# Kernel optimization log

Hardware: AMD Instinct MI355X
Metric: run time of the kernel (lower is better)

## Reference

```python
import jax, jax.numpy as jnp
import numpy as np

L, H, D, F = 6, 8, 512, 2048
B, T, S = 8, 512, 1024
DK = D // H


def setup_inputs() -> dict:
    key = jax.random.key(0)
    ks = jax.random.split(key, 16)
    p = lambda k, shape: jax.random.normal(k, shape, jnp.float32) * 0.02
    inp = {
        "tgt": jax.random.normal(ks[0], (B, T, D), jnp.float32),
        "memory": jax.random.normal(ks[1], (B, S, D), jnp.float32),
        "source_mask": jnp.ones((B, 1, 1, S), jnp.int32),
        "target_mask": jnp.broadcast_to(jnp.tril(jnp.ones((T, T), jnp.int32)), (B, 1, T, T)),
        # self-attention params, stacked over layers
        "sa_wq": p(ks[2], (L, D, D)), "sa_wk": p(ks[3], (L, D, D)),
        "sa_wv": p(ks[4], (L, D, D)), "sa_wo": p(ks[5], (L, D, D)),
        "sa_bq": jnp.zeros((L, D)), "sa_bk": jnp.zeros((L, D)),
        "sa_bv": jnp.zeros((L, D)), "sa_bo": jnp.zeros((L, D)),
        # cross-attention params
        "ca_wq": p(ks[6], (L, D, D)), "ca_wk": p(ks[7], (L, D, D)),
        "ca_wv": p(ks[8], (L, D, D)), "ca_wo": p(ks[9], (L, D, D)),
        "ca_bq": jnp.zeros((L, D)), "ca_bk": jnp.zeros((L, D)),
        "ca_bv": jnp.zeros((L, D)), "ca_bo": jnp.zeros((L, D)),
        # FFN params
        "ff_w1": p(ks[10], (L, D, F)), "ff_b1": jnp.zeros((L, F)),
        "ff_w2": p(ks[11], (L, F, D)), "ff_b2": jnp.zeros((L, D)),
        # single shared LayerNorm (as in the original module)
        "ln_g": jnp.ones((D,)), "ln_b": jnp.zeros((D,)),
    }
    return inp


def _layernorm(x, g, b, eps=1e-5):
    m = jnp.mean(x, axis=-1, keepdims=True)
    v = jnp.var(x, axis=-1, keepdims=True)
    return (x - m) * jax.lax.rsqrt(v + eps) * g + b


def _mha(xq, xk, xv, wq, bq, wk, bk, wv, bv, wo, bo, mask):
    Bq = xq.shape[0]
    proj = lambda x, w, b: (x @ w + b).reshape(Bq, -1, H, DK).transpose(0, 2, 1, 3)
    q, k, v = proj(xq, wq, bq), proj(xk, wk, bk), proj(xv, wv, bv)  # [B,H,*,DK]
    scores = jnp.einsum('bhtd,bhsd->bhts', q, k) / jnp.sqrt(jnp.float32(DK))
    scores = jnp.where(mask == 0, jnp.float32(-1e9), scores)
    p_attn = jax.nn.softmax(scores, axis=-1)
    o = jnp.einsum('bhts,bhsd->bhtd', p_attn, v)
    o = o.transpose(0, 2, 1, 3).reshape(Bq, -1, H * DK)
    return o @ wo + bo


def reference(tgt, memory, source_mask, target_mask,
              sa_wq, sa_wk, sa_wv, sa_wo, sa_bq, sa_bk, sa_bv, sa_bo,
              ca_wq, ca_wk, ca_wv, ca_wo, ca_bq, ca_bk, ca_bv, ca_bo,
              ff_w1, ff_b1, ff_w2, ff_b2, ln_g, ln_b):
    output = tgt
    for i in range(L):
        # NOTE: faithful to original code: self-attn block uses `tgt`, not `output`
        n = _layernorm(tgt, ln_g, ln_b)
        output = tgt + _mha(n, n, n,
                            sa_wq[i], sa_bq[i], sa_wk[i], sa_bk[i],
                            sa_wv[i], sa_bv[i], sa_wo[i], sa_bo[i], target_mask)
        n = _layernorm(output, ln_g, ln_b)
        output = output + _mha(n, memory, memory,
                               ca_wq[i], ca_bq[i], ca_wk[i], ca_bk[i],
                               ca_wv[i], ca_bv[i], ca_wo[i], ca_bo[i], source_mask)
        n = _layernorm(output, ln_g, ln_b)
        ff = jax.nn.relu(n @ ff_w1[i] + ff_b1[i]) @ ff_w2[i] + ff_b2[i]
        output = output + ff
    return _layernorm(output, ln_g, ln_b)
```

## Files before the change

kernel.cpp:

```cpp
#include <hip/hip_runtime.h>

typedef __bf16 bf16;
typedef unsigned short u16;
typedef __bf16 bf16x8 __attribute__((ext_vector_type(8)));
typedef __bf16 bf16x4 __attribute__((ext_vector_type(4)));
typedef float f32x4 __attribute__((ext_vector_type(4)));

#define GLL16(gp, lp)                                                        \
    __builtin_amdgcn_global_load_lds(                                        \
        (const __attribute__((address_space(1))) void*)(gp),                 \
        (__attribute__((address_space(3))) void*)(lp), 16, 0, 0)

__device__ __forceinline__ bool is_f32(const void* lng_raw) {
    return ((const unsigned int*)lng_raw)[0] == 0x3F800000u;
}

__device__ __forceinline__ float ldf(const void* base, size_t idx, bool f32) {
    return f32 ? ((const float*)base)[idx] : (float)((const bf16*)base)[idx];
}

__device__ __forceinline__ uint4 load8(const void* base, size_t idx, bool f) {
    if (!f) return *(const uint4*)((const bf16*)base + idx);
    const float* p = (const float*)base + idx;
    float4 a = ((const float4*)p)[0], b = ((const float4*)p)[1];
    union { uint4 u; bf16 h[8]; } r;
    r.h[0] = (bf16)a.x; r.h[1] = (bf16)a.y; r.h[2] = (bf16)a.z; r.h[3] = (bf16)a.w;
    r.h[4] = (bf16)b.x; r.h[5] = (bf16)b.y; r.h[6] = (bf16)b.z; r.h[7] = (bf16)b.w;
    return r.u;
}

struct SrcList { const void* p[10]; };
struct DstList { u16* p[10]; };
struct VecList { const void* p[12]; };
__global__ __launch_bounds__(256) void prep_all_k(SrcList SL, DstList DL, VecList VL,
                                                  bf16* __restrict__ cvec,
                                                  const void* __restrict__ mem,
                                                  bf16* __restrict__ membf,
                                                  const void* __restrict__ tgt,
                                                  bf16* __restrict__ nbuf) {
    __shared__ u16 tile[32][33];
    const void* lng_raw = VL.p[10];
    const void* lnb_raw = VL.p[11];
    bool f = is_f32(lng_raw);
    int bid = blockIdx.x;
    int tid = threadIdx.x;
    if (bid < 4096) {
        int t = bid;
        int widx, R, C, tile_id;
        if (t < 2048) { widx = t >> 8; R = 512; C = 512; tile_id = t & 255; }
        else if (t < 3072) { widx = 8; R = 512; C = 2048; tile_id = t - 2048; }
        else { widx = 9; R = 2048; C = 512; tile_id = t - 3072; }
        int tpr = C >> 5;
        int cx = (tile_id % tpr) * 32, ry = (tile_id / tpr) * 32;
        size_t off = (widx < 8) ? (size_t)5 * 512 * 512 : (size_t)5 * 512 * 2048;
        const void* src = SL.p[widx];
        u16* dst = DL.p[widx];
        int tx = tid & 31, ty = tid >> 5;
#pragma unroll
        for (int i = 0; i < 32; i += 8) {
            bf16 bv = (bf16)ldf(src, off + (size_t)(ry + ty + i) * C + cx + tx, f);
            tile[ty + i][tx] = *(u16*)&bv;
        }
        __syncthreads();
        int a = tid >> 3, b0 = (tid & 7) * 4;
        __align__(8) u16 o4[4];
#pragma unroll
        for (int j = 0; j < 4; ++j) o4[j] = tile[b0 + j][a];
        *(uint2*)&dst[(size_t)(cx + a) * R + ry + b0] = *(const uint2*)o4;
    } else if (bid < 4126) {
        int i = (bid - 4096) * 256 + tid;
        const int L5D = 5 * 512, L5F = 5 * 2048;
        float v;
        if (i < 512) v = ldf(VL.p[0], L5D + i, f);
        else if (i < 1024) v = ldf(VL.p[1], L5D + i - 512, f);
        else if (i < 1536) v = ldf(VL.p[2], L5D + i - 1024, f);
        else if (i < 2048) v = ldf(VL.p[5], L5D + i - 1536, f);
        else if (i < 2560) v = ldf(VL.p[6], L5D + i - 2048, f);
        else if (i < 3072) v = ldf(VL.p[3], L5D + i - 2560, f);
        else if (i < 3584) v = ldf(VL.p[4], L5D + i - 3072, f);
        else if (i < 4096) v = ldf(VL.p[7], L5D + i - 3584, f);
        else if (i < 6144) v = ldf(VL.p[8], L5F + i - 4096, f);
        else if (i < 6656) v = ldf(VL.p[9], L5D + i - 6144, f);
        else if (i < 7168) v = ldf(VL.p[10], i - 6656, f);
        else v = ldf(VL.p[11], i - 7168, f);
        cvec[i] = (bf16)v;
    } else if (bid < 6174) {
        size_t i = ((size_t)(bid - 4126) * 256 + tid) * 8;
        *(uint4*)(membf + i) = load8(mem, i, f);
    } else {
        int row = (bid - 6174) * 4 + (tid >> 6);
        int lane = tid & 63;
        size_t base = (size_t)row * 512 + lane * 8;
        float v[8];
        if (f) {
            const float* xr = (const float*)tgt + base;
            float4 a = ((const float4*)xr)[0], b2 = ((const float4*)xr)[1];
            v[0] = a.x; v[1] = a.y; v[2] = a.z; v[3] = a.w;
            v[4] = b2.x; v[5] = b2.y; v[6] = b2.z; v[7] = b2.w;
        } else {
            uint4 u = *(const uint4*)((const bf16*)tgt + base);
            const bf16* p = (const bf16*)&u;
#pragma unroll
            for (int i = 0; i < 8; ++i) v[i] = (float)p[i];
        }
        float s = 0.f, s2 = 0.f;
#pragma unroll
        for (int i = 0; i < 8; ++i) { s += v[i]; s2 += v[i] * v[i]; }
#pragma unroll
        for (int off = 32; off >= 1; off >>= 1) {
            s += __shfl_xor(s, off);
            s2 += __shfl_xor(s2, off);
        }
        float mean = s * (1.f / 512.f);
        float var = fmaxf(s2 * (1.f / 512.f) - mean * mean, 0.f);
        float rstd = rsqrtf(var + 1e-5f);
        int col = lane * 8;
        uint4 gu = load8(lng_raw, col, f);
        uint4 bu = load8(lnb_raw, col, f);
        const bf16* gp = (const bf16*)&gu;
        const bf16* bp = (const bf16*)&bu;
        __align__(16) bf16 o8[8];
#pragma unroll
        for (int i = 0; i < 8; ++i)
            o8[i] = (bf16)((v[i] - mean) * rstd * (float)gp[i] + (float)bp[i]);
        *(uint4*)(nbuf + (size_t)row * 512 + col) = *(const uint4*)o8;
    }
}

__global__ __launch_bounds__(256) void vt2_k(const bf16* __restrict__ qkv,
                                             const bf16* __restrict__ kvca,
                                             bf16* __restrict__ vt_sa,
                                             bf16* __restrict__ vt_ca) {
    __shared__ u16 tile[32][33];
    int bid = blockIdx.x;
    const u16* src;
    u16* dst;
    int S, ld, coff, xs, ys, bh;
    if (bid < 2048) {
        src = (const u16*)qkv; dst = (u16*)vt_sa; S = 512; ld = 1536; coff = 1024;
        xs = bid & 15; ys = (bid >> 4) & 1; bh = bid >> 5;
    } else {
        int t = bid - 2048;
        src = (const u16*)kvca; dst = (u16*)vt_ca; S = 1024; ld = 1024; coff = 512;
        xs = t & 31; ys = (t >> 5) & 1; bh = t >> 6;
    }
    int b = bh >> 3, h = bh & 7;
    int s0 = xs * 32, d0 = ys * 32;
    int tx = threadIdx.x & 31, ty = threadIdx.x >> 5;
#pragma unroll
    for (int i = 0; i < 32; i += 8)
        tile[ty + i][tx] = src[(size_t)(b * S + s0 + ty + i) * ld + coff + h * 64 + d0 + tx];
    __syncthreads();
    int a = threadIdx.x >> 3, b0 = (threadIdx.x & 7) * 4;
    __align__(8) u16 o4[4];
#pragma unroll
    for (int j = 0; j < 4; ++j) o4[j] = tile[b0 + j][a];
    *(uint2*)&dst[((size_t)bh * 64 + d0 + a) * S + s0 + b0] = *(const uint2*)o4;
}

template <typename TIN>
__global__ __launch_bounds__(256) void ln_kernel(const TIN* __restrict__ x,
                                                 bf16* __restrict__ out,
                                                 const bf16* __restrict__ g,
                                                 const bf16* __restrict__ bb) {
    int row = blockIdx.x * 4 + (threadIdx.x >> 6);
    int lane = threadIdx.x & 63;
    const TIN* xr = x + (size_t)row * 512 + lane * 8;
    float v[8];
    if constexpr (sizeof(TIN) == 2) {
        uint4 u = *(const uint4*)xr;
        const bf16* p = (const bf16*)&u;
#pragma unroll
        for (int i = 0; i < 8; ++i) v[i] = (float)p[i];
    } else {
        float4 a = ((const float4*)xr)[0];
        float4 b2 = ((const float4*)xr)[1];
        v[0] = a.x; v[1] = a.y; v[2] = a.z; v[3] = a.w;
        v[4] = b2.x; v[5] = b2.y; v[6] = b2.z; v[7] = b2.w;
    }
    float s = 0.f, s2 = 0.f;
#pragma unroll
    for (int i = 0; i < 8; ++i) { s += v[i]; s2 += v[i] * v[i]; }
#pragma unroll
    for (int off = 32; off >= 1; off >>= 1) {
        s += __shfl_xor(s, off);
        s2 += __shfl_xor(s2, off);
    }
    float mean = s * (1.f / 512.f);
    float var = fmaxf(s2 * (1.f / 512.f) - mean * mean, 0.f);
    float rstd = rsqrtf(var + 1e-5f);
    int col = lane * 8;
    __align__(16) bf16 o8[8];
#pragma unroll
    for (int i = 0; i < 8; ++i)
        o8[i] = (bf16)((v[i] - mean) * rstd * (float)g[col + i] + (float)bb[col + i]);
    *(uint4*)(out + (size_t)row * 512 + col) = *(const uint4*)o8;
}

__global__ __launch_bounds__(256) void ln_final_k(const float* __restrict__ x,
                                                  void* __restrict__ out,
                                                  const bf16* __restrict__ g,
                                                  const bf16* __restrict__ bb,
                                                  const void* __restrict__ lng_raw) {
    int row = blockIdx.x * 4 + (threadIdx.x >> 6);
    int lane = threadIdx.x & 63;
    const float* xr = x + (size_t)row * 512 + lane * 8;
    float v[8];
    float4 a = ((const float4*)xr)[0];
    float4 b2 = ((const float4*)xr)[1];
    v[0] = a.x; v[1] = a.y; v[2] = a.z; v[3] = a.w;
    v[4] = b2.x; v[5] = b2.y; v[6] = b2.z; v[7] = b2.w;
    float s = 0.f, s2 = 0.f;
#pragma unroll
    for (int i = 0; i < 8; ++i) { s += v[i]; s2 += v[i] * v[i]; }
#pragma unroll
    for (int off = 32; off >= 1; off >>= 1) {
        s += __shfl_xor(s, off);
        s2 += __shfl_xor(s2, off);
    }
    float mean = s * (1.f / 512.f);
    float var = fmaxf(s2 * (1.f / 512.f) - mean * mean, 0.f);
    float rstd = rsqrtf(var + 1e-5f);
    int col = lane * 8;
    float o[8];
#pragma unroll
    for (int i = 0; i < 8; ++i)
        o[i] = (v[i] - mean) * rstd * (float)g[col + i] + (float)bb[col + i];
    if (is_f32(lng_raw)) {
        float* op = (float*)out + (size_t)row * 512 + col;
        ((float4*)op)[0] = make_float4(o[0], o[1], o[2], o[3]);
        ((float4*)op)[1] = make_float4(o[4], o[5], o[6], o[7]);
    } else {
        __align__(16) bf16 o8[8];
#pragma unroll
        for (int i = 0; i < 8; ++i) o8[i] = (bf16)o[i];
        *(uint4*)((bf16*)out + (size_t)row * 512 + col) = *(const uint4*)o8;
    }
}

template <int TM, int TN, int RES, bool RELU, int DB, typename OUT_T>
__device__ __forceinline__ void gemm_body(const bf16* A, const bf16* Bt, const bf16* bias,
                                          const void* res, OUT_T* C,
                                          int K, int lda, int ldc,
                                          int m0, int n0, bool fR, bf16* lA, bf16* lB) {
    constexpr int MI = TM / 32;
    constexpr int NI = TN / 32;
    constexpr int APASS = TM / 32;
    constexpr int BPASS = TN / 32;
    int tid = threadIdx.x;
    int w = tid >> 6, lane = tid & 63, quad = lane >> 4, c = lane & 15;
    int wm = (w >> 1) * (TM / 2), wn = (w & 1) * (TN / 2);
    f32x4 acc[MI][NI] = {};

    auto issue = [&](int kt, int bs) {
        bf16* dA = lA + bs * (TM * 64);
        bf16* dB = lB + bs * (TN * 64);
#pragma unroll
        for (int r = 0; r < BPASS; ++r) {
            int id = r * 256 + tid;
            int rw = id >> 3, ch = id & 7;
            int sc = ch ^ (rw & 7);
            GLL16(&Bt[(size_t)(n0 + rw) * K + kt + sc * 8], &dB[id * 8]);
        }
#pragma unroll
        for (int r = 0; r < APASS; ++r) {
            int id = r * 256 + tid;
            int rw = id >> 3, ch = id & 7;
            int sc = ch ^ (rw & 7);
            GLL16(&A[(size_t)(m0 + rw) * lda + kt + sc * 8], &dA[id * 8]);
        }
    };
    auto fragread = [&](int bs, bf16x8 af[MI][2], bf16x8 bfr[NI][2]) {
        bf16* sA = lA + bs * (TM * 64);
        bf16* sB = lB + bs * (TN * 64);
#pragma unroll
        for (int i = 0; i < MI; ++i) {
            int row = wm + i * 16 + c;
#pragma unroll
            for (int kk = 0; kk < 2; ++kk)
                af[i][kk] = *(const bf16x8*)&sA[row * 64 + (((kk * 4 + quad) ^ (row & 7)) << 3)];
        }
#pragma unroll
        for (int i = 0; i < NI; ++i) {
            int row = wn + i * 16 + c;
#pragma unroll
            for (int kk = 0; kk < 2; ++kk)
                bfr[i][kk] = *(const bf16x8*)&sB[row * 64 + (((kk * 4 + quad) ^ (row & 7)) << 3)];
        }
    };

    issue(0, 0);
    __syncthreads();
    int cur = 0;
    for (int kt = 0; kt < K; kt += 64) {
        bf16x8 af[MI][2], bfr[NI][2];
        if (DB == 0) {
            fragread(0, af, bfr);
            __syncthreads();
            if (kt + 64 < K) issue(kt + 64, 0);
            __builtin_amdgcn_sched_barrier(0);
        } else {
            if (kt + 64 < K) issue(kt + 64, cur ^ 1);
            __builtin_amdgcn_sched_barrier(0);
            fragread(cur, af, bfr);
        }
#pragma unroll
        for (int kk = 0; kk < 2; ++kk)
#pragma unroll
            for (int mi = 0; mi < MI; ++mi)
#pragma unroll
                for (int ni = 0; ni < NI; ++ni)
                    acc[mi][ni] = __builtin_amdgcn_mfma_f32_16x16x32_bf16(
                        af[mi][kk], bfr[ni][kk], acc[mi][ni], 0, 0, 0);
        __syncthreads();
        cur ^= 1;
    }

#pragma unroll
    for (int mi = 0; mi < MI; ++mi) {
#pragma unroll
        for (int ni = 0; ni < NI; ++ni) {
#pragma unroll
            for (int r = 0; r < 4; ++r) {
                int row = m0 + wm + mi * 16 + quad * 4 + r;
                int col = n0 + wn + ni * 16 + c;
                float v = acc[mi][ni][r] + (float)bias[col];
                if (RELU) v = fmaxf(v, 0.f);
                if (RES == 1) v += ldf(res, (size_t)row * 512 + col, fR);
                if (RES == 2) v += ((const float*)res)[(size_t)row * 512 + col];
                C[(size_t)row * ldc + col] = (OUT_T)v;
            }
        }
    }
}

__global__ __launch_bounds__(256) void gemm_qkv_cakv(const bf16* __restrict__ nbuf,
                                                     const bf16* __restrict__ membf,
                                                     const bf16* __restrict__ wqkv,
                                                     const bf16* __restrict__ wcakv,
                                                     const bf16* __restrict__ cvec,
                                                     bf16* __restrict__ qkv,
                                                     bf16* __restrict__ kvca) {
    __shared__ __align__(16) bf16 lA[128 * 64];
    __shared__ __align__(16) bf16 lB[64 * 64];
    int bid = blockIdx.x;
    const bf16* A; const bf16* Bt; const bf16* bias; bf16* C;
    int ldc, m0, n0;
    if (bid < 768) {
        A = nbuf; Bt = wqkv; bias = cvec; C = qkv; ldc = 1536;
        m0 = (bid & 31) * 128; n0 = (bid >> 5) * 64;
    } else {
        int t = bid - 768;
        A = membf; Bt = wcakv; bias = cvec + 1536; C = kvca; ldc = 1024;
        m0 = (t & 63) * 128; n0 = (t >> 6) * 64;
    }
    gemm_body<128, 64, 0, false, 0, bf16>(A, Bt, bias, nullptr, C, 512, 512, ldc,
                                          m0, n0, false, lA, lB);
}

template <int TM, int TN, int RES, bool RELU, int DB, typename OUT_T>
__global__ __launch_bounds__(256) void gemmN(const bf16* __restrict__ A,
                                             const bf16* __restrict__ Bt,
                                             const bf16* __restrict__ bias,
                                             const void* __restrict__ res,
                                             OUT_T* __restrict__ C,
                                             int K, int lda, int ldc,
                                             const void* __restrict__ lng_raw) {
    __shared__ __align__(16) bf16 lA[(DB + 1) * TM * 64];
    __shared__ __align__(16) bf16 lB[(DB + 1) * TN * 64];
    bool f = (RES == 1) ? is_f32(lng_raw) : false;
    gemm_body<TM, TN, RES, RELU, DB, OUT_T>(A, Bt, bias, res, C, K, lda, ldc,
                                            blockIdx.x * TM, blockIdx.y * TN, f, lA, lB);
}

__global__ __launch_bounds__(256) void lngemm_k(const float* __restrict__ x,
                                                const bf16* __restrict__ Bt,
                                                const bf16* __restrict__ bias,
                                                const bf16* __restrict__ lng,
                                                const bf16* __restrict__ lnb,
                                                bf16* __restrict__ C, int ldc) {
    __shared__ __align__(16) bf16 lA[2 * 64 * 32];
    __shared__ __align__(16) bf16 lB[2 * 64 * 32];
    __shared__ float sm[64], sr[64];
    const int K = 512;
    int tid = threadIdx.x;
    int m0 = blockIdx.x * 64, n0 = blockIdx.y * 64;
    int w = tid >> 6, lane = tid & 63, quad = lane >> 4, c = lane & 15;
    int wm = (w >> 1) * 32, wn = (w & 1) * 32;

#pragma unroll 4
    for (int rr = 0; rr < 16; ++rr) {
        const float* xr = x + (size_t)(m0 + w * 16 + rr) * 512 + lane * 8;
        float4 a = ((const float4*)xr)[0], b2 = ((const float4*)xr)[1];
        float s = a.x + a.y + a.z + a.w + b2.x + b2.y + b2.z + b2.w;
        float s2 = a.x * a.x + a.y * a.y + a.z * a.z + a.w * a.w +
                   b2.x * b2.x + b2.y * b2.y + b2.z * b2.z + b2.w * b2.w;
#pragma unroll
        for (int off = 32; off >= 1; off >>= 1) {
            s += __shfl_xor(s, off);
            s2 += __shfl_xor(s2, off);
        }
        if (lane == 0) {
            float mean = s * (1.f / 512.f);
            float var = fmaxf(s2 * (1.f / 512.f) - mean * mean, 0.f);
            sm[w * 16 + rr] = mean;
            sr[w * 16 + rr] = rsqrtf(var + 1e-5f);
        }
    }
    __syncthreads();

    int rw = tid >> 2, ch = tid & 3;
    int swA = rw * 32 + ((ch ^ ((rw >> 1) & 3)) << 3);
    float amean = sm[rw], arstd = sr[rw];
    f32x4 acc[2][2] = {};
    float4 a0, a1;

    auto loadA = [&](int kt) {
        const float* p = x + (size_t)(m0 + rw) * 512 + kt + ch * 8;
        a0 = ((const float4*)p)[0];
        a1 = ((const float4*)p)[1];
    };
    auto issueB = [&](int kt, int bs) {
        int sc = ch ^ ((rw >> 1) & 3);
        GLL16(&Bt[(size_t)(n0 + rw) * K + kt + sc * 8], &lB[bs * (64 * 32) + tid * 8]);
    };
    auto writeA = [&](int kt, int bs) {
        uint4 gu = *(const uint4*)(lng + kt + ch * 8);
        uint4 bu = *(const uint4*)(lnb + kt + ch * 8);
        const bf16* gp = (const bf16*)&gu;
        const bf16* bp = (const bf16*)&bu;
        float vv[8] = {a0.x, a0.y, a0.z, a0.w, a1.x, a1.y, a1.z, a1.w};
        __align__(16) bf16 o8[8];
#pragma unroll
        for (int i = 0; i < 8; ++i)
            o8[i] = (bf16)((vv[i] - amean) * arstd * (float)gp[i] + (float)bp[i]);
        *(uint4*)&lA[bs * (64 * 32) + swA] = *(const uint4*)o8;
    };

    loadA(0);
    issueB(0, 0);
    writeA(0, 0);
    __syncthreads();
    int cur = 0;
    for (int kt = 0; kt < K; kt += 32) {
        bool more = kt + 32 < K;
        if (more) { loadA(kt + 32); issueB(kt + 32, cur ^ 1); }
        __builtin_amdgcn_sched_barrier(0);
        bf16* sA = lA + cur * (64 * 32);
        bf16* sB = lB + cur * (64 * 32);
        bf16x8 af[2], bfr[2];
#pragma unroll
        for (int i = 0; i < 2; ++i) {
            int row = wm + i * 16 + c;
            af[i] = *(const bf16x8*)&sA[row * 32 + ((quad ^ ((row >> 1) & 3)) << 3)];
        }
#pragma unroll
        for (int i = 0; i < 2; ++i) {
            int row = wn + i * 16 + c;
            bfr[i] = *(const bf16x8*)&sB[row * 32 + ((quad ^ ((row >> 1) & 3)) << 3)];
        }
#pragma unroll
        for (int mi = 0; mi < 2; ++mi)
#pragma unroll
            for (int ni = 0; ni < 2; ++ni)
                acc[mi][ni] = __builtin_amdgcn_mfma_f32_16x16x32_bf16(
                    af[mi], bfr[ni], acc[mi][ni], 0, 0, 0);
        if (more) writeA(kt + 32, cur ^ 1);
        __syncthreads();
        cur ^= 1;
    }

#pragma unroll
    for (int mi = 0; mi < 2; ++mi) {
#pragma unroll
        for (int ni = 0; ni < 2; ++ni) {
#pragma unroll
            for (int r = 0; r < 4; ++r) {
                int row = m0 + wm + mi * 16 + quad * 4 + r;
                int col = n0 + wn + ni * 16 + c;
                C[(size_t)row * ldc + col] = (bf16)(acc[mi][ni][r] + (float)bias[col]);
            }
        }
    }
}

template <bool CAUSAL>
__global__ __launch_bounds__(256) void attn2_k(const bf16* __restrict__ Qb, int ldq,
                                               const bf16* __restrict__ Kb, int ldk,
                                               const bf16* __restrict__ Vt,
                                               const int* __restrict__ smask,
                                               bf16* __restrict__ O, int ldo,
                                               int Tq, int Skv) {
    __shared__ __align__(16) bf16 QPs[64 * 64];
    __shared__ __align__(16) bf16 Ks[2][64 * 64];
    __shared__ __align__(16) bf16 Vts[2][64 * 64];
    int tid = threadIdx.x;
    int bh = blockIdx.x;
    int b = bh >> 3, h = bh & 7;
    int hoff = h * 64;
    int w = tid >> 6, lane = tid & 63, quad = lane >> 4, c = lane & 15;

    auto issueKV = [&](int j, int bs) {
        int kbase = j * 64;
#pragma unroll
        for (int rr = 0; rr < 2; ++rr) {
            int id = rr * 256 + tid;
            int rw = id >> 3, ch = id & 7;
            int sg = (ch ^ (rw & 7)) << 3;
            GLL16(&Kb[(size_t)(b * Skv + kbase + rw) * ldk + hoff + sg], &Ks[bs][id * 8]);
            GLL16(&Vt[((size_t)bh * 64 + rw) * Skv + kbase + sg], &Vts[bs][id * 8]);
        }
    };

    int nt = CAUSAL ? 2 : 1;
    for (int t = 0; t < nt; ++t) {
        int qt = CAUSAL ? (t ? 7 - (int)blockIdx.y : (int)blockIdx.y) : (int)blockIdx.y;
        int qbase = qt * 64;
        int nkb = CAUSAL ? (qt + 1) : (Skv >> 6);
        int qg = qbase + w * 16 + c;

        if (t) __syncthreads();
#pragma unroll
        for (int rr = 0; rr < 2; ++rr) {
            int id = rr * 256 + tid;
            int rw = id >> 3, ch = id & 7;
            *(uint4*)&QPs[rw * 64 + ((ch ^ (rw & 7)) << 3)] =
                *(const uint4*)&Qb[(size_t)(b * Tq + qbase + rw) * ldq + hoff + ch * 8];
        }
        issueKV(0, 0);
        __syncthreads();
        bf16x8 qf[2];
        {
            int row = w * 16 + c;
            qf[0] = *(const bf16x8*)&QPs[row * 64 + ((quad ^ (row & 7)) << 3)];
            qf[1] = *(const bf16x8*)&QPs[row * 64 + (((4 + quad) ^ (row & 7)) << 3)];
        }

        float m_st = -1e4f, l_st = 0.f;
        f32x4 o_acc[4] = {};
        char* Pw = (char*)(QPs + w * 1024);

        int cur = 0;
        for (int j = 0; j < nkb; ++j) {
            int kbase = j * 64;
            if (j + 1 < nkb) issueKV(j + 1, cur ^ 1);
            __builtin_amdgcn_sched_barrier(0);
            const bf16* K_ = Ks[cur];
            const bf16* V_ = Vts[cur];

            f32x4 sv[4] = {};
#pragma unroll
            for (int ni = 0; ni < 4; ++ni) {
                int row = ni * 16 + c;
#pragma unroll
                for (int kk = 0; kk < 2; ++kk) {
                    bf16x8 kf = *(const bf16x8*)&K_[row * 64 + ((((kk << 2) + quad) ^ (row & 7)) << 3)];
                    sv[ni] = __builtin_amdgcn_mfma_f32_16x16x32_bf16(kf, qf[kk], sv[ni], 0, 0, 0);
                }
            }

            float vv[4][4];
            float rm = -1e4f;
#pragma unroll
            for (int ni = 0; ni < 4; ++ni) {
                int kv0 = kbase + ni * 16 + quad * 4;
                if (CAUSAL) {
#pragma unroll
                    for (int r = 0; r < 4; ++r) {
                        vv[ni][r] = (kv0 + r <= qg) ? sv[ni][r] * 0.125f : -1e4f;
                        rm = fmaxf(rm, vv[ni][r]);
                    }
                } else {
                    int4 mk = *(const int4*)&smask[b * Skv + kv0];
                    const int* mp = (const int*)&mk;
#pragma unroll
                    for (int r = 0; r < 4; ++r) {
                        vv[ni][r] = mp[r] ? sv[ni][r] * 0.125f : -1e4f;
                        rm = fmaxf(rm, vv[ni][r]);
                    }
                }
            }
            rm = fmaxf(rm, __shfl_xor(rm, 16));
            rm = fmaxf(rm, __shfl_xor(rm, 32));
            float mn = fmaxf(m_st, rm);
            float alpha = __expf(m_st - mn);
            float rs = 0.f;
#pragma unroll
            for (int ni = 0; ni < 4; ++ni) {
                __align__(8) bf16 p4[4];
#pragma unroll
                for (int r = 0; r < 4; ++r) {
                    float p = (vv[ni][r] > -9.9e3f) ? __expf(vv[ni][r] - mn) : 0.f;
                    rs += p;
                    p4[r] = (bf16)p;
                }
                int g = ni * 2 + (quad >> 1);
                *(bf16x4*)(Pw + c * 128 + ((g ^ (c & 7)) << 4) + (quad & 1) * 8) =
                    *(const bf16x4*)p4;
            }
            rs += __shfl_xor(rs, 16);
            rs += __shfl_xor(rs, 32);
            l_st = l_st * alpha + rs;
            m_st = mn;
#pragma unroll
            for (int dt = 0; dt < 4; ++dt)
#pragma unroll
                for (int r = 0; r < 4; ++r) o_acc[dt][r] *= alpha;

            bf16x8 pf[2];
            pf[0] = *(const bf16x8*)(Pw + c * 128 + ((quad ^ (c & 7)) << 4));
            pf[1] = *(const bf16x8*)(Pw + c * 128 + (((4 + quad) ^ (c & 7)) << 4));
#pragma unroll
            for (int dt = 0; dt < 4; ++dt) {
                int row = dt * 16 + c;
#pragma unroll
                for (int kk = 0; kk < 2; ++kk) {
                    bf16x8 vf = *(const bf16x8*)&V_[row * 64 + ((((kk << 2) + quad) ^ (row & 7)) << 3)];
                    o_acc[dt] = __builtin_amdgcn_mfma_f32_16x16x32_bf16(vf, pf[kk], o_acc[dt], 0, 0, 0);
                }
            }
            __syncthreads();
            cur ^= 1;
        }

        float inv = 1.f / fmaxf(l_st, 1e-20f);
        size_t orow = (size_t)(b * Tq + qbase + w * 16 + c);
#pragma unroll
        for (int dt = 0; dt < 4; ++dt) {
            __align__(8) bf16 o4[4];
#pragma unroll
            for (int r = 0; r < 4; ++r) o4[r] = (bf16)(o_acc[dt][r] * inv);
            *(bf16x4*)&O[orow * ldo + hoff + dt * 16 + quad * 4] = *(const bf16x4*)o4;
        }
    }
}

extern "C" void kernel_launch(void* const* d_in, const int* in_sizes, int n_in,
                              void* d_out, int out_size, void* d_ws, size_t ws_size,
                              hipStream_t stream) {
    (void)in_sizes; (void)n_in; (void)out_size; (void)ws_size;
    const size_t DD = (size_t)512 * 512;
    const int* smask = (const int*)d_in[2];
    const void* lng_raw = d_in[24];

    char* ws = (char*)d_ws;
    size_t off = 0;
    auto alloc = [&](size_t bytes) { void* p = ws + off; off += (bytes + 255) & ~(size_t)255; return p; };
    bf16* wt_qkv = (bf16*)alloc(1536 * 512 * 2);
    bf16* wt_sao = (bf16*)alloc(512 * 512 * 2);
    bf16* wt_caq = (bf16*)alloc(512 * 512 * 2);
    bf16* wt_cakv = (bf16*)alloc(1024 * 512 * 2);
    bf16* wt_cao = (bf16*)alloc(512 * 512 * 2);
    bf16* wt_ff1 = (bf16*)alloc(2048 * 512 * 2);
    bf16* wt_ff2 = (bf16*)alloc(512 * 2048 * 2);
    bf16* cvec = (bf16*)alloc(7680 * 2);
    bf16* membf = (bf16*)alloc((size_t)8192 * 512 * 2);
    bf16* nbuf = (bf16*)alloc((size_t)4096 * 512 * 2);
    bf16* attn = (bf16*)alloc((size_t)4096 * 512 * 2);
    bf16* qca = (bf16*)alloc((size_t)4096 * 512 * 2);
    float* x = (float*)alloc((size_t)4096 * 512 * 4);
    bf16* vt_sa = (bf16*)alloc((size_t)64 * 64 * 512 * 2);
    bf16* vt_ca = (bf16*)alloc((size_t)64 * 64 * 1024 * 2);
    bf16* kvca = (bf16*)alloc((size_t)8192 * 1024 * 2);
    bf16* big = (bf16*)alloc((size_t)4096 * 2048 * 2);
    bf16* qkv = big;
    bf16* hbuf = big;

    SrcList SL; DstList DL; VecList VL;
    SL.p[0] = d_in[4];  DL.p[0] = (u16*)wt_qkv;
    SL.p[1] = d_in[5];  DL.p[1] = (u16*)(wt_qkv + DD);
    SL.p[2] = d_in[6];  DL.p[2] = (u16*)(wt_qkv + 2 * DD);
    SL.p[3] = d_in[7];  DL.p[3] = (u16*)wt_sao;
    SL.p[4] = d_in[12]; DL.p[4] = (u16*)wt_caq;
    SL.p[5] = d_in[13]; DL.p[5] = (u16*)wt_cakv;
    SL.p[6] = d_in[14]; DL.p[6] = (u16*)(wt_cakv + DD);
    SL.p[7] = d_in[15]; DL.p[7] = (u16*)wt_cao;
    SL.p[8] = d_in[20]; DL.p[8] = (u16*)wt_ff1;
    SL.p[9] = d_in[22]; DL.p[9] = (u16*)wt_ff2;
    VL.p[0] = d_in[8];  VL.p[1] = d_in[9];  VL.p[2] = d_in[10]; VL.p[3] = d_in[11];
    VL.p[4] = d_in[16]; VL.p[5] = d_in[17]; VL.p[6] = d_in[18]; VL.p[7] = d_in[19];
    VL.p[8] = d_in[21]; VL.p[9] = d_in[23]; VL.p[10] = d_in[24]; VL.p[11] = d_in[25];

    const bf16* lng = cvec + 6656;
    const bf16* lnb = cvec + 7168;

    prep_all_k<<<7198, 256, 0, stream>>>(SL, DL, VL, cvec, d_in[1], membf,
                                         d_in[0], nbuf);
    gemm_qkv_cakv<<<1792, 256, 0, stream>>>(nbuf, membf, wt_qkv, wt_cakv, cvec,
                                            qkv, kvca);
    vt2_k<<<6144, 256, 0, stream>>>(qkv, kvca, vt_sa, vt_ca);

    attn2_k<true><<<dim3(64, 4), 256, 0, stream>>>(
        qkv, 1536, qkv + 512, 1536, vt_sa, nullptr, attn, 512, 512, 512);
    gemmN<64, 64, 1, false, 1, float><<<dim3(64, 8), 256, 0, stream>>>(
        attn, wt_sao, cvec + 2560, d_in[0], x, 512, 512, 512, lng_raw);

    lngemm_k<<<dim3(64, 8), 256, 0, stream>>>(x, wt_caq, cvec + 3072,
                                              lng, lnb, qca, 512);
    attn2_k<false><<<dim3(64, 8), 256, 0, stream>>>(
        qca, 512, kvca, 1024, vt_ca, smask, attn, 512, 512, 1024);
    gemmN<64, 64, 2, false, 1, float><<<dim3(64, 8), 256, 0, stream>>>(
        attn, wt_cao, cvec + 3584, x, x, 512, 512, 512, lng_raw);

    ln_kernel<float><<<1024, 256, 0, stream>>>(x, nbuf, lng, lnb);
    gemmN<128, 64, 0, true, 0, bf16><<<dim3(32, 32), 256, 0, stream>>>(
        nbuf, wt_ff1, cvec + 4096, nullptr, hbuf, 512, 512, 2048, lng_raw);
    gemmN<64, 64, 2, false, 1, float><<<dim3(64, 8), 256, 0, stream>>>(
        hbuf, wt_ff2, cvec + 6144, x, x, 2048, 2048, 512, lng_raw);

    ln_final_k<<<1024, 256, 0, stream>>>(x, d_out, lng, lnb, lng_raw);
}
```

Before: 326.4 us.

## Fuse FFN layernorm into FF1 GEMM and fold cross-attn V transpose into causal attention

Templates the layernorm-fused GEMM on tile width and ReLU so the FFN pre-norm and first FFN GEMM run as one kernel, removing the separate layernorm launch and the bf16 normalized-activation round trip. It also moves the cross-attention V transpose out of the transpose kernel and into extra blocks of the causal self-attention launch, so that transpose work can overlap with attention. The trade-off is that the FF1 GEMM now recomputes row statistics per block and uses a smaller K tile than the previous dedicated GEMM. The attention grid is also flattened, which mixes the small transpose blocks with the heavy attention blocks.

```diff
diff --git a/kernel.cpp b/kernel.cpp
--- a/kernel.cpp
+++ b/kernel.cpp
@@ -158,45 +158,6 @@
     *(uint2*)&dst[((size_t)bh * 64 + d0 + a) * S + s0 + b0] = *(const uint2*)o4;
 }
 
-template <typename TIN>
-__global__ __launch_bounds__(256) void ln_kernel(const TIN* __restrict__ x,
-                                                 bf16* __restrict__ out,
-                                                 const bf16* __restrict__ g,
-                                                 const bf16* __restrict__ bb) {
-    int row = blockIdx.x * 4 + (threadIdx.x >> 6);
-    int lane = threadIdx.x & 63;
-    const TIN* xr = x + (size_t)row * 512 + lane * 8;
-    float v[8];
-    if constexpr (sizeof(TIN) == 2) {
-        uint4 u = *(const uint4*)xr;
-        const bf16* p = (const bf16*)&u;
-#pragma unroll
-        for (int i = 0; i < 8; ++i) v[i] = (float)p[i];
-    } else {
-        float4 a = ((const float4*)xr)[0];
-        float4 b2 = ((const float4*)xr)[1];
-        v[0] = a.x; v[1] = a.y; v[2] = a.z; v[3] = a.w;
-        v[4] = b2.x; v[5] = b2.y; v[6] = b2.z; v[7] = b2.w;
-    }
-    float s = 0.f, s2 = 0.f;
-#pragma unroll
-    for (int i = 0; i < 8; ++i) { s += v[i]; s2 += v[i] * v[i]; }
-#pragma unroll
-    for (int off = 32; off >= 1; off >>= 1) {
-        s += __shfl_xor(s, off);
-        s2 += __shfl_xor(s2, off);
-    }
-    float mean = s * (1.f / 512.f);
-    float var = fmaxf(s2 * (1.f / 512.f) - mean * mean, 0.f);
-    float rstd = rsqrtf(var + 1e-5f);
-    int col = lane * 8;
-    __align__(16) bf16 o8[8];
-#pragma unroll
-    for (int i = 0; i < 8; ++i)
-        o8[i] = (bf16)((v[i] - mean) * rstd * (float)g[col + i] + (float)bb[col + i]);
-    *(uint4*)(out + (size_t)row * 512 + col) = *(const uint4*)o8;
-}
-
 __global__ __launch_bounds__(256) void ln_final_k(const float* __restrict__ x,
                                                   void* __restrict__ out,
                                                   const bf16* __restrict__ g,
@@ -373,20 +334,23 @@
                                             blockIdx.x * TM, blockIdx.y * TN, f, lA, lB);
 }
 
+template <int TN, bool RELU>
 __global__ __launch_bounds__(256) void lngemm_k(const float* __restrict__ x,
                                                 const bf16* __restrict__ Bt,
                                                 const bf16* __restrict__ bias,
                                                 const bf16* __restrict__ lng,
                                                 const bf16* __restrict__ lnb,
                                                 bf16* __restrict__ C, int ldc) {
+    constexpr int NI = TN / 32;
+    constexpr int BPASS = TN / 64;
     __shared__ __align__(16) bf16 lA[2 * 64 * 32];
-    __shared__ __align__(16) bf16 lB[2 * 64 * 32];
+    __shared__ __align__(16) bf16 lB[2 * TN * 32];
     __shared__ float sm[64], sr[64];
     const int K = 512;
     int tid = threadIdx.x;
-    int m0 = blockIdx.x * 64, n0 = blockIdx.y * 64;
+    int m0 = blockIdx.x * 64, n0 = blockIdx.y * TN;
     int w = tid >> 6, lane = tid & 63, quad = lane >> 4, c = lane & 15;
-    int wm = (w >> 1) * 32, wn = (w & 1) * 32;
+    int wm = (w >> 1) * 32, wn = (w & 1) * (TN / 2);
 
 #pragma unroll 4
     for (int rr = 0; rr < 16; ++rr) {
@@ -412,7 +376,7 @@
     int rw = tid >> 2, ch = tid & 3;
     int swA = rw * 32 + ((ch ^ ((rw >> 1) & 3)) << 3);
     float amean = sm[rw], arstd = sr[rw];
-    f32x4 acc[2][2] = {};
+    f32x4 acc[2][NI] = {};
     float4 a0, a1;
 
     auto loadA = [&](int kt) {
@@ -421,8 +385,13 @@
         a1 = ((const float4*)p)[1];
     };
     auto issueB = [&](int kt, int bs) {
-        int sc = ch ^ ((rw >> 1) & 3);
-        GLL16(&Bt[(size_t)(n0 + rw) * K + kt + sc * 8], &lB[bs * (64 * 32) + tid * 8]);
+#pragma unroll
+        for (int r = 0; r < BPASS; ++r) {
+            int id = r * 256 + tid;
+            int brw = id >> 2, bch = id & 3;
+            int sc = bch ^ ((brw >> 1) & 3);
+            GLL16(&Bt[(size_t)(n0 + brw) * K + kt + sc * 8], &lB[bs * (TN * 32) + id * 8]);
+        }
     };
     auto writeA = [&](int kt, int bs) {
         uint4 gu = *(const uint4*)(lng + kt + ch * 8);
@@ -447,22 +416,22 @@
         if (more) { loadA(kt + 32); issueB(kt + 32, cur ^ 1); }
         __builtin_amdgcn_sched_barrier(0);
         bf16* sA = lA + cur * (64 * 32);
-        bf16* sB = lB + cur * (64 * 32);
-        bf16x8 af[2], bfr[2];
+        bf16* sB = lB + cur * (TN * 32);
+        bf16x8 af[2], bfr[NI];
 #pragma unroll
         for (int i = 0; i < 2; ++i) {
             int row = wm + i * 16 + c;
             af[i] = *(const bf16x8*)&sA[row * 32 + ((quad ^ ((row >> 1) & 3)) << 3)];
         }
 #pragma unroll
-        for (int i = 0; i < 2; ++i) {
+        for (int i = 0; i < NI; ++i) {
             int row = wn + i * 16 + c;
             bfr[i] = *(const bf16x8*)&sB[row * 32 + ((quad ^ ((row >> 1) & 3)) << 3)];
         }
 #pragma unroll
         for (int mi = 0; mi < 2; ++mi)
 #pragma unroll
-            for (int ni = 0; ni < 2; ++ni)
+            for (int ni = 0; ni < NI; ++ni)
                 acc[mi][ni] = __builtin_amdgcn_mfma_f32_16x16x32_bf16(
                     af[mi], bfr[ni], acc[mi][ni], 0, 0, 0);
         if (more) writeA(kt + 32, cur ^ 1);
@@ -473,12 +442,14 @@
 #pragma unroll
     for (int mi = 0; mi < 2; ++mi) {
 #pragma unroll
-        for (int ni = 0; ni < 2; ++ni) {
+        for (int ni = 0; ni < NI; ++ni) {
 #pragma unroll
             for (int r = 0; r < 4; ++r) {
                 int row = m0 + wm + mi * 16 + quad * 4 + r;
                 int col = n0 + wn + ni * 16 + c;
-                C[(size_t)row * ldc + col] = (bf16)(acc[mi][ni][r] + (float)bias[col]);
+                float v = acc[mi][ni][r] + (float)bias[col];
+                if (RELU) v = fmaxf(v, 0.f);
+                C[(size_t)row * ldc + col] = (bf16)v;
             }
         }
     }
@@ -490,12 +461,39 @@
                                                const bf16* __restrict__ Vt,
                                                const int* __restrict__ smask,
                                                bf16* __restrict__ O, int ldo,
-                                               int Tq, int Skv) {
+                                               int Tq, int Skv,
+                                               const bf16* __restrict__ kvca_t,
+                                               bf16* __restrict__ vtca) {
     __shared__ __align__(16) bf16 QPs[64 * 64];
     __shared__ __align__(16) bf16 Ks[2][64 * 64];
     __shared__ __align__(16) bf16 Vts[2][64 * 64];
     int tid = threadIdx.x;
-    int bh = blockIdx.x;
+    int bid = blockIdx.x;
+
+    if (CAUSAL && bid >= 256) {
+        u16(*tile)[33] = (u16(*)[33])QPs;
+        int t = bid - 256;
+        const u16* src = (const u16*)kvca_t;
+        u16* dst = (u16*)vtca;
+        int xs = t & 31, ys = (t >> 5) & 1, bh2 = t >> 6;
+        int b2 = bh2 >> 3, h2 = bh2 & 7;
+        int s0 = xs * 32, d0 = ys * 32;
+        int tx = tid & 31, ty = tid >> 5;
+#pragma unroll
+        for (int i = 0; i < 32; i += 8)
+            tile[ty + i][tx] =
+                src[(size_t)(b2 * 1024 + s0 + ty + i) * 1024 + 512 + h2 * 64 + d0 + tx];
+        __syncthreads();
+        int a = tid >> 3, b0 = (tid & 7) * 4;
+        __align__(8) u16 o4[4];
+#pragma unroll
+        for (int j = 0; j < 4; ++j) o4[j] = tile[b0 + j][a];
+        *(uint2*)&dst[((size_t)bh2 * 64 + d0 + a) * 1024 + s0 + b0] = *(const uint2*)o4;
+        return;
+    }
+
+    int bh = bid & 63;
+    int yq = bid >> 6;
     int b = bh >> 3, h = bh & 7;
     int hoff = h * 64;
     int w = tid >> 6, lane = tid & 63, quad = lane >> 4, c = lane & 15;
@@ -514,7 +512,7 @@
 
     int nt = CAUSAL ? 2 : 1;
     for (int t = 0; t < nt; ++t) {
-        int qt = CAUSAL ? (t ? 7 - (int)blockIdx.y : (int)blockIdx.y) : (int)blockIdx.y;
+        int qt = CAUSAL ? (t ? 7 - yq : yq) : yq;
         int qbase = qt * 64;
         int nkb = CAUSAL ? (qt + 1) : (Skv >> 6);
         int qg = qbase + w * 16 + c;
@@ -688,23 +686,24 @@
                                          d_in[0], nbuf);
     gemm_qkv_cakv<<<1792, 256, 0, stream>>>(nbuf, membf, wt_qkv, wt_cakv, cvec,
                                             qkv, kvca);
-    vt2_k<<<6144, 256, 0, stream>>>(qkv, kvca, vt_sa, vt_ca);
-
-    attn2_k<true><<<dim3(64, 4), 256, 0, stream>>>(
-        qkv, 1536, qkv + 512, 1536, vt_sa, nullptr, attn, 512, 512, 512);
+    vt2_k<<<2048, 256, 0, stream>>>(qkv, kvca, vt_sa, vt_ca);
+
+    attn2_k<true><<<4352, 256, 0, stream>>>(
+        qkv, 1536, qkv + 512, 1536, vt_sa, nullptr, attn, 512, 512, 512,
+        kvca, vt_ca);
     gemmN<64, 64, 1, false, 1, float><<<dim3(64, 8), 256, 0, stream>>>(
         attn, wt_sao, cvec + 2560, d_in[0], x, 512, 512, 512, lng_raw);
 
-    lngemm_k<<<dim3(64, 8), 256, 0, stream>>>(x, wt_caq, cvec + 3072,
-                                              lng, lnb, qca, 512);
-    attn2_k<false><<<dim3(64, 8), 256, 0, stream>>>(
-        qca, 512, kvca, 1024, vt_ca, smask, attn, 512, 512, 1024);
+    lngemm_k<64, false><<<dim3(64, 8), 256, 0, stream>>>(x, wt_caq, cvec + 3072,
+                                                         lng, lnb, qca, 512);
+    attn2_k<false><<<512, 256, 0, stream>>>(
+        qca, 512, kvca, 1024, vt_ca, smask, attn, 512, 512, 1024,
+        nullptr, nullptr);
     gemmN<64, 64, 2, false, 1, float><<<dim3(64, 8), 256, 0, stream>>>(
         attn, wt_cao, cvec + 3584, x, x, 512, 512, 512, lng_raw);
 
-    ln_kernel<float><<<1024, 256, 0, stream>>>(x, nbuf, lng, lnb);
-    gemmN<128, 64, 0, true, 0, bf16><<<dim3(32, 32), 256, 0, stream>>>(
-        nbuf, wt_ff1, cvec + 4096, nullptr, hbuf, 512, 512, 2048, lng_raw);
+    lngemm_k<128, true><<<dim3(64, 16), 256, 0, stream>>>(x, wt_ff1, cvec + 4096,
+                                                          lng, lnb, hbuf, 2048);
     gemmN<64, 64, 2, false, 1, float><<<dim3(64, 8), 256, 0, stream>>>(
         hbuf, wt_ff2, cvec + 6144, x, x, 2048, 2048, 512, lng_raw);
 
```

New measurement: 335.9 us. +2.9%, slower.
